# Performance work log

Hardware: AMD Instinct MI355X
Metric: run time of the kernel (lower is better)

## Reference

```python
import jax, jax.numpy as jnp
import numpy as np

NUM_CAMS = 1
NUM_HEADS = 1
NUM_LEVELS = 1
NUM_POINTS = 4
NUM_DEPTH = 128
EMBED = 128  # must equal NUM_DEPTH (output_proj is applied to the depth axis)


def setup_inputs() -> dict:
    key0 = jax.random.key(0)
    ks = jax.random.split(key0, 12)
    bsv, nq, nv = 1, 1024, 1024  # nq == nv == H*W (32*32)
    off_dim = NUM_CAMS * NUM_HEADS * NUM_LEVELS * NUM_DEPTH * NUM_POINTS * 2  # 1024
    aw_dim = NUM_CAMS * NUM_HEADS * NUM_LEVELS * NUM_DEPTH * NUM_POINTS       # 512
    return {
        "query": jax.random.normal(ks[0], (bsv, nq, EMBED), jnp.float32),
        "key": jax.random.normal(ks[1], (NUM_CAMS, nv, bsv, EMBED), jnp.float32),
        "value": jax.random.normal(ks[2], (NUM_CAMS, nv, bsv, EMBED), jnp.float32),
        "ref_3d": jax.random.uniform(ks[3], (bsv * NUM_CAMS, nq * NUM_DEPTH, 2), jnp.float32),
        "spatial_shapes": jnp.array([[32, 32]], dtype=jnp.int32),
        "W_off": jax.random.normal(ks[4], (EMBED, off_dim), jnp.float32) * 0.02,
        "b_off": jax.random.normal(ks[5], (off_dim,), jnp.float32) * 0.02,
        "W_attn": jax.random.normal(ks[6], (EMBED, aw_dim), jnp.float32) * 0.02,
        "b_attn": jax.random.normal(ks[7], (aw_dim,), jnp.float32) * 0.02,
        "W_v": jax.random.normal(ks[8], (EMBED, EMBED), jnp.float32) / np.sqrt(EMBED),
        "b_v": jnp.zeros((EMBED,), jnp.float32),
        "W_o": jax.random.normal(ks[9], (EMBED, EMBED), jnp.float32) / np.sqrt(EMBED),
        "b_o": jnp.zeros((EMBED,), jnp.float32),
    }


def _bilinear_sample(val, H, W, x, y):
    """grid_sample(align_corners=False, padding=zeros) equivalent.
    val: [B, H*W, D]; x, y: [B, Q, P] in pixel coords. Returns [B, Q, P, D]."""
    B, Q, P = x.shape
    D = val.shape[-1]
    x0f = jnp.floor(x); y0f = jnp.floor(y)
    ix0 = x0f.astype(jnp.int32); iy0 = y0f.astype(jnp.int32)
    wx1 = x - x0f; wy1 = y - y0f
    wx0 = 1.0 - wx1; wy0 = 1.0 - wy1

    def corner(ix, iy, w):
        valid = (ix >= 0) & (ix < W) & (iy >= 0) & (iy < H)
        idx = jnp.clip(iy, 0, H - 1) * W + jnp.clip(ix, 0, W - 1)  # [B,Q,P]
        g = jnp.take_along_axis(val, idx.reshape(B, Q * P)[:, :, None], axis=1)
        g = g.reshape(B, Q, P, D)
        return g * (w * valid.astype(val.dtype))[..., None]

    return (corner(ix0, iy0, wx0 * wy0)
            + corner(ix0 + 1, iy0, wx1 * wy0)
            + corner(ix0, iy0 + 1, wx0 * wy1)
            + corner(ix0 + 1, iy0 + 1, wx1 * wy1))


def reference(query, key, value, ref_3d, spatial_shapes,
              W_off, b_off, W_attn, b_attn, W_v, b_v, W_o, b_o):
    bsv, nq, E = query.shape
    cams, nv, bs, _ = key.shape
    identity = query

    # key/value: [cams, nv, bs, E] -> [bsv, nv, E]
    key2 = jnp.transpose(key, (2, 0, 1, 3)).reshape(bsv, nv, E)
    val = jnp.flip(value, axis=0)
    val = jnp.transpose(val, (2, 0, 1, 3)).reshape(bsv, nv, E)
    val = val @ W_v + b_v
    val = val.reshape(bsv * cams, nv, E)  # num_heads=1 -> head_dim=E

    # offsets / attention weights (heads=levels=1 axes squeezed)
    off = (query @ W_off + b_off).reshape(bsv, nq, cams, NUM_DEPTH, NUM_POINTS, 2)
    aw = (query @ W_attn + b_attn).reshape(bsv, nq, cams, NUM_DEPTH, NUM_LEVELS * NUM_POINTS)
    aw = jax.nn.softmax(aw, axis=-1).reshape(bsv, nq, cams, NUM_DEPTH, NUM_POINTS)
    off = jnp.transpose(off, (0, 2, 1, 3, 4, 5)).reshape(bsv * cams, nq * NUM_DEPTH, NUM_POINTS, 2)
    aw = jnp.transpose(aw, (0, 2, 1, 3, 4)).reshape(bsv * cams, nq * NUM_DEPTH, NUM_POINTS)

    H = spatial_shapes[0, 0]
    W = spatial_shapes[0, 1]
    norm = jnp.stack([W, H]).astype(off.dtype)  # [W, H]
    loc = ref_3d[:, :, None, :] + off / norm    # [B, Qe, P, 2] in [0,1]
    x = loc[..., 0] * W.astype(loc.dtype) - 0.5
    y = loc[..., 1] * H.astype(loc.dtype) - 0.5

    sampled = _bilinear_sample(val, H, W, x, y)          # [B, Qe, P, E]
    out = jnp.einsum('bqpe,bqp->bqe', sampled, aw)       # weighted sum over points

    out = out.reshape(bsv, cams, nq, NUM_DEPTH, E).mean(axis=1)  # [bsv, nq, depth, E]
    out = (out * key2[:, :, None, :]).mean(axis=-1)              # [bsv, nq, depth]
    out = out @ W_o + b_o                                        # depth == EMBED
    return out + identity  # dropout = identity in eval
```

## Files before the change

### kernel.cpp

```cpp
#include <hip/hip_runtime.h>


#define NQ   1024
#define NV   1024
#define ND   128
#define NP   4
#define IMG_W 32
#define IMG_H 32
#define QB   4

typedef __attribute__((ext_vector_type(8))) short bfx8;
typedef __attribute__((ext_vector_type(4))) float f32x4;

__device__ __forceinline__ unsigned short bf_rne(float f) {
  unsigned u = __float_as_uint(f);
  return (unsigned short)((u + 0x7FFFu + ((u >> 16) & 1u)) >> 16);
}
__device__ __forceinline__ float bf2f(unsigned short u) {
  return __uint_as_float((unsigned)u << 16);
}
__device__ __forceinline__ bfx8 pack8(const float* p) {
  bfx8 v;
#pragma unroll
  for (int j = 0; j < 8; ++j) v[j] = (short)bf_rne(p[j]);
  return v;
}

__global__ __launch_bounds__(512) void mono_kernel(
    const float* __restrict__ query, const float* __restrict__ key,
    const float* __restrict__ value, const float* __restrict__ ref3d,
    const float* __restrict__ W_off, const float* __restrict__ b_off,
    const float* __restrict__ W_attn, const float* __restrict__ b_attn,
    const float* __restrict__ W_v, const float* __restrict__ b_v,
    const float* __restrict__ W_o, const float* __restrict__ b_o,
    float* __restrict__ out) {
  __shared__ float q_lds[QB][128];
  __shared__ float key_lds[QB][128];
  __shared__ float keyp_lds[QB][128];
  __shared__ float c_lds[QB];
  __shared__ unsigned short img_bf[QB][NV];
  __shared__ unsigned short off_bf[QB][1024];
  __shared__ unsigned short aw_bf[QB][512];
  __shared__ __align__(16) unsigned short sval[128 * 128];
  float* o1s = (float*)sval;

  const int tid = threadIdx.x;
  const int q0 = blockIdx.x * QB;
  const int w = tid >> 6, l = tid & 63;
  const int col = l & 15, g = l >> 4;

  if (tid < 128) {
    ((float4*)q_lds)[tid] = ((const float4*)(query + (size_t)q0 * 128))[tid];
  } else if (tid < 256) {
    ((float4*)key_lds)[tid - 128] =
        ((const float4*)(key + (size_t)q0 * 128))[tid - 128];
  }
#pragma unroll
  for (int it = 0; it < 4; ++it) {
    const int c = tid + it * 512;
    const int r = c >> 4, cc = c & 15;
    const bfx8 v = pack8(W_v + (size_t)r * 128 + cc * 8);
    const int byte = r * 256 + ((cc * 16) ^ ((r & 15) << 4));
    *(bfx8*)((char*)sval + byte) = v;
  }
  __syncthreads();

  {
    bfx8 afK[4];
#pragma unroll
    for (int ks = 0; ks < 4; ++ks) {
      bfx8 a;
      if (col < QB) {
        a = pack8(&key_lds[col][ks * 32 + g * 8]);
      } else {
#pragma unroll
        for (int j = 0; j < 8; ++j) a[j] = 0;
      }
      afK[ks] = a;
    }
    {
      const int r = w * 16 + col;
      f32x4 acc = {0.f, 0.f, 0.f, 0.f};
#pragma unroll
      for (int ks = 0; ks < 4; ++ks) {
        const int colb = (ks * 64 + g * 16) ^ (col << 4);
        const bfx8 bfr = *(const bfx8*)((const char*)sval + r * 256 + colb);
        acc = __builtin_amdgcn_mfma_f32_16x16x32_bf16(afK[ks], bfr, acc,
                                                      0, 0, 0);
      }
      if (g == 0) {
#pragma unroll
        for (int i = 0; i < QB; ++i) keyp_lds[i][r] = acc[i];
      }
    }
    if (tid < QB) {
      float s = 0.f;
      for (int e = 0; e < 128; e += 4) {
        const float4 bv = *(const float4*)(b_v + e);
        const float4 k4 = *(const float4*)(&key_lds[tid][e]);
        s = fmaf(bv.x, k4.x,
            fmaf(bv.y, k4.y, fmaf(bv.z, k4.z, fmaf(bv.w, k4.w, s))));
      }
      c_lds[tid] = s;
    }
  }
  __syncthreads();

  if (w < 4) {
    const int t = tid;
    float4 aoff[QB];
    float2 aaw[QB];
#pragma unroll
    for (int qq = 0; qq < QB; ++qq) {
      aoff[qq] = make_float4(0.f, 0.f, 0.f, 0.f);
      aaw[qq] = make_float2(0.f, 0.f);
    }
    const float* wo_p = W_off + (size_t)t * 4;
    const float* wa_p = W_attn + (size_t)t * 2;
#pragma unroll 4
    for (int e4 = 0; e4 < 32; ++e4) {
      float4 q4[QB];
#pragma unroll
      for (int qq = 0; qq < QB; ++qq)
        q4[qq] = *(const float4*)(&q_lds[qq][e4 * 4]);
#pragma unroll
      for (int j = 0; j < 4; ++j) {
        const int e = e4 * 4 + j;
        const float4 w4 = *(const float4*)(wo_p + (size_t)e * 1024);
        const float2 w2 = *(const float2*)(wa_p + (size_t)e * 512);
#pragma unroll
        for (int qq = 0; qq < QB; ++qq) {
          const float* qp = (const float*)&q4[qq];
          const float qv = qp[j];
          aoff[qq].x = fmaf(qv, w4.x, aoff[qq].x);
          aoff[qq].y = fmaf(qv, w4.y, aoff[qq].y);
          aoff[qq].z = fmaf(qv, w4.z, aoff[qq].z);
          aoff[qq].w = fmaf(qv, w4.w, aoff[qq].w);
          aaw[qq].x = fmaf(qv, w2.x, aaw[qq].x);
          aaw[qq].y = fmaf(qv, w2.y, aaw[qq].y);
        }
      }
    }
    const float4 bo4 = *(const float4*)(b_off + t * 4);
    const float2 ba2 = *(const float2*)(b_attn + t * 2);
#pragma unroll
    for (int qq = 0; qq < QB; ++qq) {
      const unsigned lo = (unsigned)bf_rne(aoff[qq].x + bo4.x) |
                          ((unsigned)bf_rne(aoff[qq].y + bo4.y) << 16);
      const unsigned hi = (unsigned)bf_rne(aoff[qq].z + bo4.z) |
                          ((unsigned)bf_rne(aoff[qq].w + bo4.w) << 16);
      *(uint2*)(&off_bf[qq][t * 4]) = make_uint2(lo, hi);
      *(unsigned*)(&aw_bf[qq][t * 2]) =
          (unsigned)bf_rne(aaw[qq].x + ba2.x) |
          ((unsigned)bf_rne(aaw[qq].y + ba2.y) << 16);
    }
  } else {
    const int ww = w - 4;
    unsigned short* buf = sval + ww * 4096;
    bfx8 afrag[4];
#pragma unroll
    for (int ks = 0; ks < 4; ++ks) {
      bfx8 a;
      if (col < QB) {
        a = pack8(&keyp_lds[col][ks * 32 + g * 8]);
      } else {
#pragma unroll
        for (int j = 0; j < 8; ++j) a[j] = 0;
      }
      afrag[ks] = a;
    }
    float cq[QB];
#pragma unroll
    for (int i = 0; i < QB; ++i) cq[i] = c_lds[i];

    for (int sub = 0; sub < 8; ++sub) {
      const int vbase = ww * 256 + sub * 32;
#pragma unroll
      for (int it = 0; it < 8; ++it) {
        const int c = l + it * 64;
        const int r = c >> 4, cc = c & 15;
        const bfx8 v = pack8(value + (size_t)(vbase + r) * 128 + cc * 8);
        const int byte = r * 256 + ((cc * 16) ^ ((r & 15) << 4));
        *(bfx8*)((char*)buf + byte) = v;
      }
#pragma unroll
      for (int cg = 0; cg < 2; ++cg) {
        const int r = cg * 16 + col;
        f32x4 acc = {0.f, 0.f, 0.f, 0.f};
#pragma unroll
        for (int ks = 0; ks < 4; ++ks) {
          const int colb = (ks * 64 + g * 16) ^ (col << 4);
          const bfx8 bfr = *(const bfx8*)((const char*)buf + r * 256 + colb);
          acc = __builtin_amdgcn_mfma_f32_16x16x32_bf16(afrag[ks], bfr, acc,
                                                        0, 0, 0);
        }
        if (g == 0) {
          const int v = vbase + r;
#pragma unroll
          for (int i = 0; i < QB; ++i)
            img_bf[i][v] = bf_rne(acc[i] + cq[i]);
        }
      }
    }
  }
  __syncthreads();

  {
    const int qq = tid >> 7;
    const int q = q0 + qq;
    const int d = tid & 127;
    const unsigned short* im = img_bf[qq];
    const size_t qe = (size_t)q * ND + d;

    const float rx = ref3d[qe * 2 + 0];
    const float ry = ref3d[qe * 2 + 1];

    const uint2 ua = *(const uint2*)(&aw_bf[qq][d * 4]);
    const float a0 = bf2f((unsigned short)(ua.x & 0xffff));
    const float a1 = bf2f((unsigned short)(ua.x >> 16));
    const float a2 = bf2f((unsigned short)(ua.y & 0xffff));
    const float a3 = bf2f((unsigned short)(ua.y >> 16));
    const float mx = fmaxf(fmaxf(a0, a1), fmaxf(a2, a3));
    const float e0 = __expf(a0 - mx), e1 = __expf(a1 - mx),
                e2 = __expf(a2 - mx), e3 = __expf(a3 - mx);
    const float inv = 1.0f / (e0 + e1 + e2 + e3);
    const float wgt4[4] = {e0 * inv, e1 * inv, e2 * inv, e3 * inv};

    const uint4 uo = *(const uint4*)(&off_bf[qq][d * 8]);
    const unsigned ox[4] = {uo.x, uo.y, uo.z, uo.w};

    float acc = 0.0f;
#pragma unroll
    for (int p = 0; p < NP; ++p) {
      const float x = rx * (float)IMG_W + bf2f((unsigned short)(ox[p] & 0xffff)) - 0.5f;
      const float y = ry * (float)IMG_H + bf2f((unsigned short)(ox[p] >> 16)) - 0.5f;
      const float xf = floorf(x), yf = floorf(y);
      const int ix0 = (int)xf, iy0 = (int)yf;
      const float wx1 = x - xf, wy1 = y - yf;
      const float wx0 = 1.0f - wx1, wy0 = 1.0f - wy1;

      float s = 0.0f;
#pragma unroll
      for (int cy = 0; cy < 2; ++cy) {
#pragma unroll
        for (int cx = 0; cx < 2; ++cx) {
          const int ix = ix0 + cx, iy = iy0 + cy;
          const bool valid = (ix >= 0) & (ix < IMG_W) & (iy >= 0) & (iy < IMG_H);
          const int cix = min(max(ix, 0), IMG_W - 1);
          const int ciy = min(max(iy, 0), IMG_H - 1);
          const float wgt = (cx ? wx1 : wx0) * (cy ? wy1 : wy0);
          s += valid ? bf2f(im[ciy * IMG_W + cix]) * wgt : 0.0f;
        }
      }
      acc += wgt4[p] * s;
    }
    o1s[qq * ND + (tid & 127)] = acc * (1.0f / 128.0f);
  }
  __syncthreads();

  {
    const int qq = tid >> 7;
    const int n = tid & 127;
    float acc = b_o[n] + q_lds[qq][n];
#pragma unroll 8
    for (int d = 0; d < 128; ++d)
      acc = fmaf(o1s[qq * ND + d], W_o[(size_t)d * 128 + n], acc);
    out[(size_t)(q0 + qq) * 128 + n] = acc;
  }
}

extern "C" void kernel_launch(void* const* d_in, const int* in_sizes, int n_in,
                              void* d_out, int out_size, void* d_ws, size_t ws_size,
                              hipStream_t stream) {
  const float* query  = (const float*)d_in[0];
  const float* key    = (const float*)d_in[1];
  const float* value  = (const float*)d_in[2];
  const float* ref3d  = (const float*)d_in[3];
  const float* W_off  = (const float*)d_in[5];
  const float* b_off  = (const float*)d_in[6];
  const float* W_attn = (const float*)d_in[7];
  const float* b_attn = (const float*)d_in[8];
  const float* W_v    = (const float*)d_in[9];
  const float* b_v    = (const float*)d_in[10];
  const float* W_o    = (const float*)d_in[11];
  const float* b_o    = (const float*)d_in[12];
  float* out = (float*)d_out;

  mono_kernel<<<NQ / QB, 512, 0, stream>>>(query, key, value, ref3d,
                                           W_off, b_off, W_attn, b_attn,
                                           W_v, b_v, W_o, b_o, out);
}
```

Baseline: 102.0 us.

## Double block size to 1024 threads and split projection and value work across more waves

Launches 1024 threads per block instead of 512. Eight waves now share the offset/attention projection, each thread computing half as many output columns. The other eight waves split the value-projection into the key-weighted image, each handling 128 value rows instead of 256. The o1s buffer gets its own shared array and the float-to-bf16 conversion switches to the HIP intrinsic. This adds parallelism within each block but uses more registers and LDS per block, which may lower occupancy, and half the threads sit idle in the sampling and output stages.

```diff
diff --git a/kernel.cpp b/kernel.cpp
--- a/kernel.cpp
+++ b/kernel.cpp
@@ -1,4 +1,5 @@
 #include <hip/hip_runtime.h>
+#include <hip/hip_bf16.h>
 
 
 #define NQ   1024
@@ -13,8 +14,9 @@
 typedef __attribute__((ext_vector_type(4))) float f32x4;
 
 __device__ __forceinline__ unsigned short bf_rne(float f) {
-  unsigned u = __float_as_uint(f);
-  return (unsigned short)((u + 0x7FFFu + ((u >> 16) & 1u)) >> 16);
+  union { __hip_bfloat16 h; unsigned short u; } v;
+  v.h = __float2bfloat16(f);
+  return v.u;
 }
 __device__ __forceinline__ float bf2f(unsigned short u) {
   return __uint_as_float((unsigned)u << 16);
@@ -26,7 +28,7 @@
   return v;
 }
 
-__global__ __launch_bounds__(512) void mono_kernel(
+__global__ __launch_bounds__(1024, 4) void mono_kernel(
     const float* __restrict__ query, const float* __restrict__ key,
     const float* __restrict__ value, const float* __restrict__ ref3d,
     const float* __restrict__ W_off, const float* __restrict__ b_off,
@@ -41,8 +43,8 @@
   __shared__ unsigned short img_bf[QB][NV];
   __shared__ unsigned short off_bf[QB][1024];
   __shared__ unsigned short aw_bf[QB][512];
-  __shared__ __align__(16) unsigned short sval[128 * 128];
-  float* o1s = (float*)sval;
+  __shared__ float o1s[QB][128];
+  __shared__ __align__(16) unsigned short sval[8 * 4096];
 
   const int tid = threadIdx.x;
   const int q0 = blockIdx.x * QB;
@@ -56,8 +58,8 @@
         ((const float4*)(key + (size_t)q0 * 128))[tid - 128];
   }
 #pragma unroll
-  for (int it = 0; it < 4; ++it) {
-    const int c = tid + it * 512;
+  for (int it = 0; it < 2; ++it) {
+    const int c = tid + it * 1024;
     const int r = c >> 4, cc = c & 15;
     const bfx8 v = pack8(W_v + (size_t)r * 128 + cc * 8);
     const int byte = r * 256 + ((cc * 16) ^ ((r & 15) << 4));
@@ -65,7 +67,7 @@
   }
   __syncthreads();
 
-  {
+  if (w < 8) {
     bfx8 afK[4];
 #pragma unroll
     for (int ks = 0; ks < 4; ++ks) {
@@ -78,46 +80,44 @@
       }
       afK[ks] = a;
     }
-    {
-      const int r = w * 16 + col;
-      f32x4 acc = {0.f, 0.f, 0.f, 0.f};
-#pragma unroll
-      for (int ks = 0; ks < 4; ++ks) {
-        const int colb = (ks * 64 + g * 16) ^ (col << 4);
-        const bfx8 bfr = *(const bfx8*)((const char*)sval + r * 256 + colb);
-        acc = __builtin_amdgcn_mfma_f32_16x16x32_bf16(afK[ks], bfr, acc,
-                                                      0, 0, 0);
-      }
-      if (g == 0) {
-#pragma unroll
-        for (int i = 0; i < QB; ++i) keyp_lds[i][r] = acc[i];
-      }
-    }
-    if (tid < QB) {
-      float s = 0.f;
-      for (int e = 0; e < 128; e += 4) {
-        const float4 bv = *(const float4*)(b_v + e);
-        const float4 k4 = *(const float4*)(&key_lds[tid][e]);
-        s = fmaf(bv.x, k4.x,
-            fmaf(bv.y, k4.y, fmaf(bv.z, k4.z, fmaf(bv.w, k4.w, s))));
-      }
-      c_lds[tid] = s;
-    }
-  }
-  __syncthreads();
-
-  if (w < 4) {
+    const int r = w * 16 + col;
+    f32x4 acc = {0.f, 0.f, 0.f, 0.f};
+#pragma unroll
+    for (int ks = 0; ks < 4; ++ks) {
+      const int colb = (ks * 64 + g * 16) ^ (col << 4);
+      const bfx8 bfr = *(const bfx8*)((const char*)sval + r * 256 + colb);
+      acc = __builtin_amdgcn_mfma_f32_16x16x32_bf16(afK[ks], bfr, acc,
+                                                    0, 0, 0);
+    }
+    if (g == 0) {
+#pragma unroll
+      for (int i = 0; i < QB; ++i) keyp_lds[i][r] = acc[i];
+    }
+  }
+  if (tid < QB) {
+    float s = 0.f;
+    for (int e = 0; e < 128; e += 4) {
+      const float4 bv = *(const float4*)(b_v + e);
+      const float4 k4 = *(const float4*)(&key_lds[tid][e]);
+      s = fmaf(bv.x, k4.x,
+          fmaf(bv.y, k4.y, fmaf(bv.z, k4.z, fmaf(bv.w, k4.w, s))));
+    }
+    c_lds[tid] = s;
+  }
+  __syncthreads();
+
+  if (w < 8) {
     const int t = tid;
-    float4 aoff[QB];
-    float2 aaw[QB];
+    float2 aoff[QB];
+    float aaw[QB];
 #pragma unroll
     for (int qq = 0; qq < QB; ++qq) {
-      aoff[qq] = make_float4(0.f, 0.f, 0.f, 0.f);
-      aaw[qq] = make_float2(0.f, 0.f);
-    }
-    const float* wo_p = W_off + (size_t)t * 4;
-    const float* wa_p = W_attn + (size_t)t * 2;
-#pragma unroll 4
+      aoff[qq] = make_float2(0.f, 0.f);
+      aaw[qq] = 0.f;
+    }
+    const float* wo_p = W_off + (size_t)t * 2;
+    const float* wa_p = W_attn + t;
+#pragma unroll 8
     for (int e4 = 0; e4 < 32; ++e4) {
       float4 q4[QB];
 #pragma unroll
@@ -126,36 +126,28 @@
 #pragma unroll
       for (int j = 0; j < 4; ++j) {
         const int e = e4 * 4 + j;
-        const float4 w4 = *(const float4*)(wo_p + (size_t)e * 1024);
-        const float2 w2 = *(const float2*)(wa_p + (size_t)e * 512);
+        const float2 w2 = *(const float2*)(wo_p + (size_t)e * 1024);
+        const float wa = wa_p[(size_t)e * 512];
 #pragma unroll
         for (int qq = 0; qq < QB; ++qq) {
-          const float* qp = (const float*)&q4[qq];
-          const float qv = qp[j];
-          aoff[qq].x = fmaf(qv, w4.x, aoff[qq].x);
-          aoff[qq].y = fmaf(qv, w4.y, aoff[qq].y);
-          aoff[qq].z = fmaf(qv, w4.z, aoff[qq].z);
-          aoff[qq].w = fmaf(qv, w4.w, aoff[qq].w);
-          aaw[qq].x = fmaf(qv, w2.x, aaw[qq].x);
-          aaw[qq].y = fmaf(qv, w2.y, aaw[qq].y);
-        }
-      }
-    }
-    const float4 bo4 = *(const float4*)(b_off + t * 4);
-    const float2 ba2 = *(const float2*)(b_attn + t * 2);
+          const float qv = ((const float*)&q4[qq])[j];
+          aoff[qq].x = fmaf(qv, w2.x, aoff[qq].x);
+          aoff[qq].y = fmaf(qv, w2.y, aoff[qq].y);
+          aaw[qq] = fmaf(qv, wa, aaw[qq]);
+        }
+      }
+    }
+    const float2 bo2 = *(const float2*)(b_off + t * 2);
+    const float ba = b_attn[t];
 #pragma unroll
     for (int qq = 0; qq < QB; ++qq) {
-      const unsigned lo = (unsigned)bf_rne(aoff[qq].x + bo4.x) |
-                          ((unsigned)bf_rne(aoff[qq].y + bo4.y) << 16);
-      const unsigned hi = (unsigned)bf_rne(aoff[qq].z + bo4.z) |
-                          ((unsigned)bf_rne(aoff[qq].w + bo4.w) << 16);
-      *(uint2*)(&off_bf[qq][t * 4]) = make_uint2(lo, hi);
-      *(unsigned*)(&aw_bf[qq][t * 2]) =
-          (unsigned)bf_rne(aaw[qq].x + ba2.x) |
-          ((unsigned)bf_rne(aaw[qq].y + ba2.y) << 16);
+      const unsigned px = (unsigned)bf_rne(aoff[qq].x + bo2.x) |
+                          ((unsigned)bf_rne(aoff[qq].y + bo2.y) << 16);
+      *(unsigned*)(&off_bf[qq][t * 2]) = px;
+      aw_bf[qq][t] = bf_rne(aaw[qq] + ba);
     }
   } else {
-    const int ww = w - 4;
+    const int ww = w - 8;
     unsigned short* buf = sval + ww * 4096;
     bfx8 afrag[4];
 #pragma unroll
@@ -173,8 +165,8 @@
 #pragma unroll
     for (int i = 0; i < QB; ++i) cq[i] = c_lds[i];
 
-    for (int sub = 0; sub < 8; ++sub) {
-      const int vbase = ww * 256 + sub * 32;
+    for (int sub = 0; sub < 4; ++sub) {
+      const int vbase = ww * 128 + sub * 32;
 #pragma unroll
       for (int it = 0; it < 8; ++it) {
         const int c = l + it * 64;
@@ -205,7 +197,7 @@
   }
   __syncthreads();
 
-  {
+  if (tid < 512) {
     const int qq = tid >> 7;
     const int q = q0 + qq;
     const int d = tid & 127;
@@ -254,17 +246,17 @@
       }
       acc += wgt4[p] * s;
     }
-    o1s[qq * ND + (tid & 127)] = acc * (1.0f / 128.0f);
-  }
-  __syncthreads();
-
-  {
+    o1s[qq][d] = acc * (1.0f / 128.0f);
+  }
+  __syncthreads();
+
+  if (tid < 512) {
     const int qq = tid >> 7;
     const int n = tid & 127;
     float acc = b_o[n] + q_lds[qq][n];
 #pragma unroll 8
     for (int d = 0; d < 128; ++d)
-      acc = fmaf(o1s[qq * ND + d], W_o[(size_t)d * 128 + n], acc);
+      acc = fmaf(o1s[qq][d], W_o[(size_t)d * 128 + n], acc);
     out[(size_t)(q0 + qq) * 128 + n] = acc;
   }
 }
@@ -286,7 +278,7 @@
   const float* b_o    = (const float*)d_in[12];
   float* out = (float*)d_out;
 
-  mono_kernel<<<NQ / QB, 512, 0, stream>>>(query, key, value, ref3d,
-                                           W_off, b_off, W_attn, b_attn,
-                                           W_v, b_v, W_o, b_o, out);
-}
+  mono_kernel<<<NQ / QB, 1024, 0, stream>>>(query, key, value, ref3d,
+                                            W_off, b_off, W_attn, b_attn,
+                                            W_v, b_v, W_o, b_o, out);
+}
```

New measurement: 105.5 us. 1.03x slower.

## Pre-convert value and weights to swizzled bf16 in a prep kernel

Applied to the files above, without the earlier changes.

Adds a prep kernel that converts value, W_v, W_off and W_attn to bf16 once per call, storing the MFMA operands in pre-swizzled layout in workspace. The main kernel then copies these bf16 tiles directly instead of every block re-reading fp32 and packing. This halves global traffic for the redundant per-block reads and removes repeated conversion ALU work. The cost is an extra launch and reduced precision for the offset and attention weights, which were fp32 before.

```diff
diff --git a/kernel.cpp b/kernel.cpp
--- a/kernel.cpp
+++ b/kernel.cpp
@@ -1,4 +1,5 @@
 #include <hip/hip_runtime.h>
+#include <hip/hip_bf16.h>
 
 
 #define NQ   1024
@@ -9,12 +10,18 @@
 #define IMG_H 32
 #define QB   4
 
+#define WS_VAL   0
+#define WS_WV    262144
+#define WS_WOFF  294912
+#define WS_WATTN 557056
+
 typedef __attribute__((ext_vector_type(8))) short bfx8;
 typedef __attribute__((ext_vector_type(4))) float f32x4;
 
 __device__ __forceinline__ unsigned short bf_rne(float f) {
-  unsigned u = __float_as_uint(f);
-  return (unsigned short)((u + 0x7FFFu + ((u >> 16) & 1u)) >> 16);
+  union { __hip_bfloat16 h; unsigned short u; } v;
+  v.h = __float2bfloat16(f);
+  return v.u;
 }
 __device__ __forceinline__ float bf2f(unsigned short u) {
   return __uint_as_float((unsigned)u << 16);
@@ -26,14 +33,38 @@
   return v;
 }
 
+__global__ __launch_bounds__(256) void prep_kernel(
+    const float* __restrict__ value, const float* __restrict__ W_v,
+    const float* __restrict__ W_off, const float* __restrict__ W_attn,
+    char* __restrict__ ws) {
+  const int idx = blockIdx.x * 256 + threadIdx.x;
+  if (idx < 16384) {
+    const int row = idx >> 4, cc = idx & 15;
+    const bfx8 v = pack8(value + (size_t)row * 128 + cc * 8);
+    *(bfx8*)(ws + WS_VAL + row * 256 + ((cc * 16) ^ ((row & 15) << 4))) = v;
+  } else if (idx < 18432) {
+    const int j = idx - 16384;
+    const int row = j >> 4, cc = j & 15;
+    const bfx8 v = pack8(W_v + (size_t)row * 128 + cc * 8);
+    *(bfx8*)(ws + WS_WV + row * 256 + ((cc * 16) ^ ((row & 15) << 4))) = v;
+  } else if (idx < 34816) {
+    const int j = idx - 18432;
+    const bfx8 v = pack8(W_off + (size_t)j * 8);
+    *(bfx8*)(ws + WS_WOFF + (size_t)j * 16) = v;
+  } else if (idx < 43008) {
+    const int j = idx - 34816;
+    const bfx8 v = pack8(W_attn + (size_t)j * 8);
+    *(bfx8*)(ws + WS_WATTN + (size_t)j * 16) = v;
+  }
+}
+
 __global__ __launch_bounds__(512) void mono_kernel(
     const float* __restrict__ query, const float* __restrict__ key,
-    const float* __restrict__ value, const float* __restrict__ ref3d,
-    const float* __restrict__ W_off, const float* __restrict__ b_off,
-    const float* __restrict__ W_attn, const float* __restrict__ b_attn,
-    const float* __restrict__ W_v, const float* __restrict__ b_v,
+    const float* __restrict__ ref3d,
+    const float* __restrict__ b_off, const float* __restrict__ b_attn,
+    const float* __restrict__ b_v,
     const float* __restrict__ W_o, const float* __restrict__ b_o,
-    float* __restrict__ out) {
+    const char* __restrict__ ws, float* __restrict__ out) {
   __shared__ float q_lds[QB][128];
   __shared__ float key_lds[QB][128];
   __shared__ float keyp_lds[QB][128];
@@ -49,6 +80,11 @@
   const int w = tid >> 6, l = tid & 63;
   const int col = l & 15, g = l >> 4;
 
+  const char* wsval = ws + WS_VAL;
+  const char* wswv = ws + WS_WV;
+  const unsigned short* wswoff = (const unsigned short*)(ws + WS_WOFF);
+  const unsigned short* wswattn = (const unsigned short*)(ws + WS_WATTN);
+
   if (tid < 128) {
     ((float4*)q_lds)[tid] = ((const float4*)(query + (size_t)q0 * 128))[tid];
   } else if (tid < 256) {
@@ -58,10 +94,7 @@
 #pragma unroll
   for (int it = 0; it < 4; ++it) {
     const int c = tid + it * 512;
-    const int r = c >> 4, cc = c & 15;
-    const bfx8 v = pack8(W_v + (size_t)r * 128 + cc * 8);
-    const int byte = r * 256 + ((cc * 16) ^ ((r & 15) << 4));
-    *(bfx8*)((char*)sval + byte) = v;
+    *(bfx8*)((char*)sval + c * 16) = *(const bfx8*)(wswv + (size_t)c * 16);
   }
   __syncthreads();
 
@@ -115,8 +148,8 @@
       aoff[qq] = make_float4(0.f, 0.f, 0.f, 0.f);
       aaw[qq] = make_float2(0.f, 0.f);
     }
-    const float* wo_p = W_off + (size_t)t * 4;
-    const float* wa_p = W_attn + (size_t)t * 2;
+    const unsigned short* wo_p = wswoff + t * 4;
+    const unsigned short* wa_p = wswattn + t * 2;
 #pragma unroll 4
     for (int e4 = 0; e4 < 32; ++e4) {
       float4 q4[QB];
@@ -126,18 +159,23 @@
 #pragma unroll
       for (int j = 0; j < 4; ++j) {
         const int e = e4 * 4 + j;
-        const float4 w4 = *(const float4*)(wo_p + (size_t)e * 1024);
-        const float2 w2 = *(const float2*)(wa_p + (size_t)e * 512);
+        const uint2 uw = *(const uint2*)(wo_p + (size_t)e * 1024);
+        const unsigned ua = *(const unsigned*)(wa_p + (size_t)e * 512);
+        const float w0 = bf2f((unsigned short)(uw.x & 0xffff));
+        const float w1 = bf2f((unsigned short)(uw.x >> 16));
+        const float w2 = bf2f((unsigned short)(uw.y & 0xffff));
+        const float w3 = bf2f((unsigned short)(uw.y >> 16));
+        const float wa0 = bf2f((unsigned short)(ua & 0xffff));
+        const float wa1 = bf2f((unsigned short)(ua >> 16));
 #pragma unroll
         for (int qq = 0; qq < QB; ++qq) {
-          const float* qp = (const float*)&q4[qq];
-          const float qv = qp[j];
-          aoff[qq].x = fmaf(qv, w4.x, aoff[qq].x);
-          aoff[qq].y = fmaf(qv, w4.y, aoff[qq].y);
-          aoff[qq].z = fmaf(qv, w4.z, aoff[qq].z);
-          aoff[qq].w = fmaf(qv, w4.w, aoff[qq].w);
-          aaw[qq].x = fmaf(qv, w2.x, aaw[qq].x);
-          aaw[qq].y = fmaf(qv, w2.y, aaw[qq].y);
+          const float qv = ((const float*)&q4[qq])[j];
+          aoff[qq].x = fmaf(qv, w0, aoff[qq].x);
+          aoff[qq].y = fmaf(qv, w1, aoff[qq].y);
+          aoff[qq].z = fmaf(qv, w2, aoff[qq].z);
+          aoff[qq].w = fmaf(qv, w3, aoff[qq].w);
+          aaw[qq].x = fmaf(qv, wa0, aaw[qq].x);
+          aaw[qq].y = fmaf(qv, wa1, aaw[qq].y);
         }
       }
     }
@@ -175,13 +213,11 @@
 
     for (int sub = 0; sub < 8; ++sub) {
       const int vbase = ww * 256 + sub * 32;
+      const char* src = wsval + (size_t)vbase * 256;
 #pragma unroll
       for (int it = 0; it < 8; ++it) {
         const int c = l + it * 64;
-        const int r = c >> 4, cc = c & 15;
-        const bfx8 v = pack8(value + (size_t)(vbase + r) * 128 + cc * 8);
-        const int byte = r * 256 + ((cc * 16) ^ ((r & 15) << 4));
-        *(bfx8*)((char*)buf + byte) = v;
+        *(bfx8*)((char*)buf + c * 16) = *(const bfx8*)(src + (size_t)c * 16);
       }
 #pragma unroll
       for (int cg = 0; cg < 2; ++cg) {
@@ -254,7 +290,7 @@
       }
       acc += wgt4[p] * s;
     }
-    o1s[qq * ND + (tid & 127)] = acc * (1.0f / 128.0f);
+    o1s[qq * ND + d] = acc * (1.0f / 128.0f);
   }
   __syncthreads();
 
@@ -285,8 +321,10 @@
   const float* W_o    = (const float*)d_in[11];
   const float* b_o    = (const float*)d_in[12];
   float* out = (float*)d_out;
-
-  mono_kernel<<<NQ / QB, 512, 0, stream>>>(query, key, value, ref3d,
-                                           W_off, b_off, W_attn, b_attn,
-                                           W_v, b_v, W_o, b_o, out);
-}
+  char* ws = (char*)d_ws;
+
+  prep_kernel<<<168, 256, 0, stream>>>(value, W_v, W_off, W_attn, ws);
+  mono_kernel<<<NQ / QB, 512, 0, stream>>>(query, key, ref3d,
+                                           b_off, b_attn, b_v, W_o, b_o,
+                                           ws, out);
+}
```

Result: slower. 119.0 us (+16.7%).
